# Kernel optimization log

Hardware: AMD Instinct MI355X
Metric: run time of the kernel (lower is better)

## Reference

```python
import jax, jax.numpy as jnp
import numpy as np

B, T, D = 4, 8160, 1024
N, H = 8, 128            # heads, units_per_head (D == N*H)
W = 12                   # block_size
LEFT_CTX = 13            # atten_left_context
L = LEFT_CTX - 1         # left context frames beyond current position
R = 0                    # atten_right_context
C = W + L + R            # context_size = 24
CAP = 50.0               # attention_logits_soft_capping


def _timing_signal(pos, channels):
    # sinusoidal embedding, channels even (1024)
    pos = pos.astype(jnp.float32)
    nt = channels // 2
    inc = np.log(10000.0) / max(nt - 1, 1)
    inv = jnp.exp(jnp.arange(nt, dtype=jnp.float32) * -inc)
    st = pos[:, :, None] * inv[None, None, :]
    return jnp.concatenate([jnp.sin(st), jnp.cos(st)], axis=2)


def _extract_block_context(x, block_size, left, right, pad_val):
    # x: [B, T, ...] -> [B, num_blocks, context_size, ...]
    pads = [(0, 0)] * x.ndim
    pads[1] = (left, right + block_size - 1)
    xp = jnp.pad(x, pads, constant_values=jnp.asarray(pad_val, x.dtype))
    frame_len = block_size + left + right
    num_frames = (xp.shape[1] - frame_len) // block_size + 1
    idx = jnp.arange(num_frames)[:, None] * block_size + jnp.arange(frame_len)[None, :]
    return jnp.take(xp, idx, axis=1)


def _convert_to_block(x, block_size):
    b, t = x.shape[0], x.shape[1]
    nb = t // block_size  # T chosen as multiple of block_size
    return x.reshape((b, nb, block_size) + x.shape[2:])


def setup_inputs() -> dict:
    key = jax.random.key(0)
    ks = jax.random.split(key, 6)
    x = jax.random.normal(ks[0], (B, T, D), dtype=jnp.float32)
    mask = jnp.ones((B, T), dtype=bool)
    i = jnp.arange(W)[:, None]
    j = jnp.arange(C)[None, :]
    causal_valid_mask = (j >= i) & (j - i <= L + R)  # [W, C]
    s = 1.0 / np.sqrt(D)
    wq = jax.random.normal(ks[1], (D, D), dtype=jnp.float32) * s
    wk = jax.random.normal(ks[2], (D, D), dtype=jnp.float32) * s
    wv = jax.random.normal(ks[3], (D, D), dtype=jnp.float32) * s
    pos_proj = jax.random.normal(ks[4], (D, N, H), dtype=jnp.float32) * s
    return {"x": x, "mask": mask, "causal_valid_mask": causal_valid_mask,
            "wq": wq, "wk": wk, "wv": wv, "pos_proj": pos_proj}


def reference(x, mask, causal_valid_mask, wq, wk, wv, pos_proj):
    b, t, d = x.shape
    u = t // W
    q = jnp.einsum('btd,df->btf', x, wq).reshape(b, t, N, H)
    k = jnp.einsum('btd,df->btf', x, wk).reshape(b, t, N, H)
    v = jnp.einsum('btd,df->btf', x, wv).reshape(b, t, N, H)

    q_blk = _convert_to_block(q, W) * (H ** -0.5)        # [B,U,W,N,H]
    k_ctx = _extract_block_context(k, W, L, R, 0.0)      # [B,U,C,N,H]
    v_ctx = _extract_block_context(v, W, L, R, 0.0)      # [B,U,C,N,H]

    # term A+C: content logits
    term_ac = jnp.einsum('BuwNH,BucNH->BNuwc', q_blk, k_ctx)

    # term B+D: relative position logits via skew trick
    pos = jnp.arange(L, -R - 1, -1)[None, :]             # [1, L+R+1]
    sin_emb = _timing_signal(pos, D)                     # [1, L+R+1, D]
    sin_emb = jnp.einsum('fd,dnh->fnh', sin_emb[0], pos_proj)  # [F,N,H]
    term_bd = jnp.einsum('BuwNH,FNH->BNuwF', q_blk, sin_emb)   # [B,N,U,W,F]
    term_bd = jnp.pad(term_bd, ((0, 0),) * 4 + ((0, C + 1 - (L + R + 1)),))
    term_bd = term_bd.reshape(b, N, u, W * (C + 1))[:, :, :, :W * C]
    term_bd = term_bd.reshape(b, N, u, W, C)

    logits = term_ac + term_bd
    logits = CAP * jnp.tanh(logits / CAP)

    mask_ctx = _extract_block_context(mask, W, L, R, False)    # [B,U,C]
    valid = mask_ctx[:, None, :, None, :] & causal_valid_mask[None, None, None, :, :]
    logits = jnp.where(valid, logits, jnp.asarray(-1e9, logits.dtype))
    probs = jax.nn.softmax(logits, axis=-1)              # [B,N,U,W,C]

    out = jnp.einsum('BNuwc,BucNH->BuwNH', probs, v_ctx)
    return out.reshape(b, u * W, N, H)[:, :t]            # [B,T,N,H]
```

## Files before the change

kernel.cpp:

```cpp
#include <hip/hip_runtime.h>
#include <cstdint>
#include <cstddef>


typedef __bf16 bf16_t;
typedef float  floatx4 __attribute__((ext_vector_type(4)));
typedef __bf16 bf16x8  __attribute__((ext_vector_type(8)));
typedef __bf16 bf16x4  __attribute__((ext_vector_type(4)));

#define GLDS16(gp, lp)                                                        \
  __builtin_amdgcn_global_load_lds(                                           \
      (const __attribute__((address_space(1))) void*)(gp),                    \
      (__attribute__((address_space(3))) void*)(lp), 16, 0, 0)

static constexpr int kT     = 8160;
static constexpr int kM     = 4 * kT;
static constexpr int kU     = kT / 12;
static constexpr int kNC    = 3200;

__global__ __launch_bounds__(256) void convert_x(const float* __restrict__ X,
                                                 bf16_t* __restrict__ Xb) {
  const size_t i = ((size_t)blockIdx.x * 256 + threadIdx.x) * 8;
  float4 a = *(const float4*)(X + i);
  float4 b = *(const float4*)(X + i + 4);
  bf16x8 o;
  o[0] = (bf16_t)a.x; o[1] = (bf16_t)a.y; o[2] = (bf16_t)a.z; o[3] = (bf16_t)a.w;
  o[4] = (bf16_t)b.x; o[5] = (bf16_t)b.y; o[6] = (bf16_t)b.z; o[7] = (bf16_t)b.w;
  *(bf16x8*)(Xb + i) = o;
}

__global__ __launch_bounds__(512) void posemb_k(const float* __restrict__ pp,
                                                float* __restrict__ pe) {
  __shared__ float st[1024];
  __shared__ float red[4][128];
  const int d   = blockIdx.x;
  const int fc  = blockIdx.y;
  const int tid = threadIdx.x;
  const float dpos = (float)d;
  for (int i = tid; i < 1024; i += 512) {
    int idx = i & 511;
    float freq = expf(-(float)idx * (9.2103403719761836f / 511.0f));
    float a = dpos * freq;
    st[i] = (i < 512) ? sinf(a) : cosf(a);
  }
  __syncthreads();
  const int part = tid >> 7;
  const int fl   = tid & 127;
  const int f    = fc * 128 + fl;
  float acc = 0.f;
  const int dd0 = part * 256;
  for (int dd = dd0; dd < dd0 + 256; ++dd)
    acc += st[dd] * pp[(size_t)dd * 1024 + f];
  red[part][fl] = acc;
  __syncthreads();
  if (tid < 128)
    pe[(size_t)d * 1024 + f] = red[0][fl] + red[1][fl] + red[2][fl] + red[3][fl];
}

__global__ __launch_bounds__(256) void transpose_w(const float* __restrict__ Wq,
                                                   const float* __restrict__ Wk,
                                                   const float* __restrict__ Wv,
                                                   bf16_t* __restrict__ Wt) {
  __shared__ float tile[64][65];
  const int g = blockIdx.z;
  const float* W = (g == 0) ? Wq : (g == 1) ? Wk : Wv;
  bf16_t* O = Wt + (size_t)g * 1024 * 1024;
  const int k0 = blockIdx.x * 64, n0 = blockIdx.y * 64;
  const int col = threadIdx.x & 63, r4 = threadIdx.x >> 6;
#pragma unroll
  for (int i = 0; i < 16; ++i) {
    int row = i * 4 + r4;
    tile[row][col] = W[(size_t)(k0 + row) * 1024 + n0 + col];
  }
  __syncthreads();
#pragma unroll
  for (int i = 0; i < 16; ++i) {
    int row = i * 4 + r4;
    O[(size_t)(n0 + row) * 1024 + k0 + col] = (bf16_t)tile[col][row];
  }
}

__global__ __launch_bounds__(256) void pe2w(const float* __restrict__ pe,
                                            bf16_t* __restrict__ Wt) {
  const int idx = blockIdx.x;
  const int tid = threadIdx.x;
  bf16_t* out = Wt + (size_t)(3072 + idx) * 1024;
  if (idx >= 104) {
    bf16x4 z = {};
    *(bf16x4*)(out + tid * 4) = z;
    return;
  }
  const int n = idx / 13, d = idx - n * 13;
  __shared__ float peh[128];
  if (tid < 128) peh[tid] = pe[(size_t)d * 1024 + n * 128 + tid];
  __syncthreads();
  float acc[4] = {};
  const bf16_t* wb = Wt + (size_t)(n * 128) * 1024 + tid * 4;
  for (int h = 0; h < 128; ++h) {
    bf16x4 w4 = *(const bf16x4*)(wb + (size_t)h * 1024);
    float s = peh[h];
    acc[0] += s * (float)w4[0];
    acc[1] += s * (float)w4[1];
    acc[2] += s * (float)w4[2];
    acc[3] += s * (float)w4[3];
  }
  bf16x4 o;
  o[0] = (bf16_t)acc[0]; o[1] = (bf16_t)acc[1];
  o[2] = (bf16_t)acc[2]; o[3] = (bf16_t)acc[3];
  *(bf16x4*)(out + tid * 4) = o;
}

__global__ __launch_bounds__(512, 2) void qkv_gemm(const bf16_t* __restrict__ X,
                                                   const bf16_t* __restrict__ Wt,
                                                   bf16_t* __restrict__ QKV) {
  __shared__ __align__(16) bf16_t lds[8][8192];

  const int flat = blockIdx.x;
  const int work = (flat & 7) * 208 + (flat >> 3);
  const int mt = work / 13, nt = work % 13;
  const int m0 = mt * 256, n0 = nt * 256;

  const int tid  = threadIdx.x;
  const int wave = tid >> 6;
  const int lane = tid & 63;
  const int wm   = wave >> 2;
  const int wn   = wave & 3;
  const int qd   = lane >> 4;
  const int lr   = lane & 15;

  const int rr  = tid >> 3;
  const int cg8 = ((tid & 7) ^ (rr & 7)) * 8;
  const bf16_t* aP[4];
  const bf16_t* bP[4];
  {
    int r2 = m0 + 128 + rr, r3 = m0 + 192 + rr;
    aP[0] = X + (size_t)(m0 + rr) * 1024 + cg8;
    aP[1] = X + (size_t)(m0 + 64 + rr) * 1024 + cg8;
    aP[2] = X + (size_t)(r2 < kM ? r2 : 0) * 1024 + cg8;
    aP[3] = X + (size_t)(r3 < kM ? r3 : 0) * 1024 + cg8;
    int s2 = n0 + 128 + rr, s3 = n0 + 192 + rr;
    bP[0] = Wt + (size_t)(n0 + rr) * 1024 + cg8;
    bP[1] = Wt + (size_t)(n0 + 64 + rr) * 1024 + cg8;
    bP[2] = Wt + (size_t)(s2 < kNC ? s2 : 0) * 1024 + cg8;
    bP[3] = Wt + (size_t)(s3 < kNC ? s3 : 0) * 1024 + cg8;
  }

#define STAGE_A(h, t)                                                          \
  do {                                                                         \
    bf16_t* d_ = &lds[((t) & 1) * 4 + (h)][wave * 512];                        \
    GLDS16(aP[2 * (h)]     + (size_t)(t) * 64, d_);                            \
    GLDS16(aP[2 * (h) + 1] + (size_t)(t) * 64, d_ + 4096);                     \
  } while (0)
#define STAGE_B(h, t)                                                          \
  do {                                                                         \
    bf16_t* d_ = &lds[((t) & 1) * 4 + 2 + (h)][wave * 512];                    \
    GLDS16(bP[2 * (h)]     + (size_t)(t) * 64, d_);                            \
    GLDS16(bP[2 * (h) + 1] + (size_t)(t) * 64, d_ + 4096);                     \
  } while (0)

  auto frag = [&](int slot, int r, int cb) -> bf16x8 {
    uint32_t off = (uint32_t)(r * 128 + cb) ^ (uint32_t)((r & 7) << 4);
    return *(const bf16x8*)((const char*)&lds[slot][0] + off);
  };

  floatx4 acc[8][4] = {};

  STAGE_A(0, 0); STAGE_A(1, 0); STAGE_B(0, 0); STAGE_B(1, 0);
  STAGE_B(0, 1); STAGE_B(1, 1);
  asm volatile("s_waitcnt vmcnt(4)" ::: "memory");
  __builtin_amdgcn_s_barrier();

  const int aslot0 = wm;
  const int bslot0 = 2 + (wn >> 1);
  const int brow0  = (wn & 1) * 64;

#pragma unroll 2
  for (int t = 0; t < 16; ++t) {
    const int par = (t & 1) * 4;
    bf16x8 bfrag[4][2];
#pragma unroll
    for (int p = 0; p < 4; ++p) {
      if (p == 0) {
#pragma unroll
        for (int in = 0; in < 4; ++in)
#pragma unroll
          for (int k2 = 0; k2 < 2; ++k2)
            bfrag[in][k2] =
                frag(par + bslot0, brow0 + in * 16 + lr, k2 * 64 + qd * 16);
      }
      bf16x8 afrag[2][2];
#pragma unroll
      for (int i = 0; i < 2; ++i)
#pragma unroll
        for (int k2 = 0; k2 < 2; ++k2)
          afrag[i][k2] =
              frag(par + aslot0, (2 * p + i) * 16 + lr, k2 * 64 + qd * 16);

      if (p == 0)      { if (t < 15) STAGE_A(0, t + 1); }
      else if (p == 1) { if (t < 15) STAGE_A(1, t + 1); }
      else if (p == 2) { if (t < 14) STAGE_B(0, t + 2); }
      else             { if (t < 14) STAGE_B(1, t + 2); }

      if (p == 3) {
        if (t < 14) asm volatile("s_waitcnt vmcnt(4)" ::: "memory");
        else        asm volatile("s_waitcnt vmcnt(0)" ::: "memory");
      }
      __builtin_amdgcn_s_barrier();
      asm volatile("s_waitcnt lgkmcnt(0)" ::: "memory");
      __builtin_amdgcn_sched_barrier(0);

      __builtin_amdgcn_s_setprio(1);
#pragma unroll
      for (int i = 0; i < 2; ++i)
#pragma unroll
        for (int in = 0; in < 4; ++in)
#pragma unroll
          for (int k2 = 0; k2 < 2; ++k2)
            acc[2 * p + i][in] = __builtin_amdgcn_mfma_f32_16x16x32_bf16(
                afrag[i][k2], bfrag[in][k2], acc[2 * p + i][in], 0, 0, 0);
      __builtin_amdgcn_s_setprio(0);
      __builtin_amdgcn_sched_barrier(0);
      __builtin_amdgcn_s_barrier();
    }
  }
#undef STAGE_A
#undef STAGE_B

  const int mBase = m0 + wm * 128 + qd * 4;
  const int nBase = n0 + wn * 64 + lr;
  if (m0 + 256 <= kM && n0 + 256 <= kNC) {
#pragma unroll
    for (int im = 0; im < 8; ++im)
#pragma unroll
      for (int in = 0; in < 4; ++in)
#pragma unroll
        for (int r = 0; r < 4; ++r)
          QKV[(size_t)(mBase + im * 16 + r) * kNC + nBase + in * 16] =
              (bf16_t)acc[im][in][r];
  } else {
#pragma unroll
    for (int im = 0; im < 8; ++im)
#pragma unroll
      for (int in = 0; in < 4; ++in)
#pragma unroll
        for (int r = 0; r < 4; ++r) {
          int m = mBase + im * 16 + r;
          int n = nBase + in * 16;
          if (m < kM && n < kNC)
            QKV[(size_t)m * kNC + n] = (bf16_t)acc[im][in][r];
        }
  }
}

__global__ __launch_bounds__(256) void qk_soft(const bf16_t* __restrict__ QKV,
                                               float* __restrict__ Pg) {
  __shared__ __align__(16) bf16_t Ks[80 * 128];
  __shared__ float qpes[64 * 16];

  const int flat  = blockIdx.x;
  const int work  = (flat & 7) * 544 + (flat >> 3);
  const int strip = work >> 5;
  const int rest  = work & 31;
  const int n     = rest >> 2;
  const int b     = rest & 3;
  const int u0    = strip * 5;
  const int t0    = u0 * 12 - 12;
  const size_t bbase = (size_t)b * kT;
  const int bn    = b * 8 + n;
  const int tid  = threadIdx.x;
  const int mi   = tid >> 6;
  const int lane = tid & 63;
  const int qd   = lane >> 4;
  const int lr   = lane & 15;

  bf16x8 aQ[4];
  {
    int tq = u0 * 12 + mi * 16 + lr;
    if (tq > kT - 1) tq = kT - 1;
    const bf16_t* qg = QKV + (bbase + tq) * kNC + n * 128;
#pragma unroll
    for (int kk = 0; kk < 4; ++kk)
      aQ[kk] = *(const bf16x8*)(qg + kk * 32 + qd * 8);
  }

  for (int i = tid; i < 80 * 16; i += 256) {
    int row = i >> 4, ch = i & 15;
    int kt = t0 + row;
    bf16x8 k8 = {};
    if (kt >= 0 && kt < kT)
      k8 = *(const bf16x8*)(QKV + (bbase + kt) * kNC + 1024 + n * 128 + ch * 8);
    int idx = (row * 128 + ch * 8) ^ ((row & 7) << 3);
    *(bf16x8*)(Ks + idx) = k8;
  }
  for (int i = tid; i < 780; i += 256) {
    int m = i / 13, d = i - m * 13;
    qpes[m * 16 + d] =
        (float)QKV[(bbase + (u0 * 12 + m)) * kNC + 3072 + n * 13 + d];
  }
  __syncthreads();

  floatx4 sAcc[2] = {};
#pragma unroll
  for (int ci = 0; ci < 2; ++ci) {
    int krow = (mi + ci) * 16 + lr;
#pragma unroll
    for (int kk = 0; kk < 4; ++kk) {
      int idx = (krow * 128 + kk * 32 + qd * 8) ^ ((krow & 7) << 3);
      bf16x8 bK = *(const bf16x8*)(Ks + idx);
      sAcc[ci] = __builtin_amdgcn_mfma_f32_16x16x32_bf16(aQ[kk], bK, sAcc[ci], 0, 0, 0);
    }
  }

#pragma unroll
  for (int r = 0; r < 4; ++r) {
    const int m = mi * 16 + qd * 4 + r;
    float e[2];
#pragma unroll
    for (int ci = 0; ci < 2; ++ci) {
      int c = (mi + ci) * 16 + lr;
      int d = m + 12 - c;
      int kt = t0 + c;
      bool v = (d >= 0) && (d <= 12) && (kt >= 0) && (m < 60);
      int qidx = m * 16 + (v ? d : 0);
      float s = (sAcc[ci][r] + qpes[qidx]) * 0.0017677669529663689f;
      float t2 = __expf(2.0f * s);
      float th = 1.0f - 2.0f / (t2 + 1.0f);
      e[ci] = v ? __expf(50.0f * th) : 0.0f;
    }
    float sm = e[0] + e[1];
    sm += __shfl_xor(sm, 1);
    sm += __shfl_xor(sm, 2);
    sm += __shfl_xor(sm, 4);
    sm += __shfl_xor(sm, 8);
    float iv = 1.0f / sm;
#pragma unroll
    for (int ci = 0; ci < 2; ++ci) {
      int c = (mi + ci) * 16 + lr;
      int d = m + 12 - c;
      if (m < 60 && d >= 0 && d <= 12)
        Pg[((size_t)bn * kT + (u0 * 12 + m)) * 16 + d] = e[ci] * iv;
    }
  }
}

__global__ __launch_bounds__(256) void pv_k(const bf16_t* __restrict__ QKV,
                                            const float* __restrict__ Pg,
                                            float* __restrict__ OUT) {
  __shared__ float Vs[60 * 132];
  __shared__ float ps[48 * 16];

  const int flat = blockIdx.x;
  const int work = (flat & 7) * 680 + (flat >> 3);
  const int bn = work / 170, ts = work % 170;
  const int b  = bn >> 3, n = bn & 7;
  const int t1 = ts * 48;
  const size_t bbase = (size_t)b * kT;
  const int tid = threadIdx.x;

  for (int i = tid; i < 60 * 16; i += 256) {
    int r = i >> 4, ch = i & 15;
    int kt = t1 - 12 + r;
    int vo = r * 132 + ch * 8;
    if (kt < 0) {
      float4 z = {};
      *(float4*)(Vs + vo) = z; *(float4*)(Vs + vo + 4) = z;
    } else {
      bf16x8 v8 = *(const bf16x8*)(QKV + (bbase + kt) * kNC + 2048 + n * 128 + ch * 8);
      float4 vl = { (float)v8[0], (float)v8[1], (float)v8[2], (float)v8[3] };
      float4 vh = { (float)v8[4], (float)v8[5], (float)v8[6], (float)v8[7] };
      *(float4*)(Vs + vo) = vl; *(float4*)(Vs + vo + 4) = vh;
    }
  }
  if (tid < 192) {
    int r = tid >> 2, q4 = tid & 3;
    float4 p4 = *(const float4*)(Pg + ((size_t)bn * kT + t1 + r) * 16 + q4 * 4);
    *(float4*)(ps + r * 16 + q4 * 4) = p4;
  }
  __syncthreads();

  for (int i = tid; i < 48 * 32; i += 256) {
    int lt = i >> 5, c4 = i & 31;
    const float* pw = ps + lt * 16;
    float4 acc = {};
#pragma unroll
    for (int d = 0; d <= 12; ++d) {
      float pd = pw[d];
      float4 v4 = *(const float4*)(Vs + (lt + 12 - d) * 132 + c4 * 4);
      acc.x += pd * v4.x; acc.y += pd * v4.y;
      acc.z += pd * v4.z; acc.w += pd * v4.w;
    }
    *(float4*)(OUT + (bbase + t1 + lt) * 1024 + n * 128 + c4 * 4) = acc;
  }
}

extern "C" void kernel_launch(void* const* d_in, const int* in_sizes, int n_in,
                              void* d_out, int out_size, void* d_ws, size_t ws_size,
                              hipStream_t stream) {
  const float* x  = (const float*)d_in[0];
  const float* wq = (const float*)d_in[3];
  const float* wk = (const float*)d_in[4];
  const float* wv = (const float*)d_in[5];
  const float* pp = (const float*)d_in[6];

  char* ws = (char*)d_ws;
  float*  pe  = (float*)ws;
  bf16_t* Wt  = (bf16_t*)(ws + (1u << 16));
  bf16_t* Xb  = (bf16_t*)(ws + (1u << 16) + 8u * 1024 * 1024);
  bf16_t* QKV = (bf16_t*)(ws + (1u << 16) + 8u * 1024 * 1024 +
                          (size_t)kM * 1024 * 2);
  float* Pg = (float*)Xb;
  float* out = (float*)d_out;

  convert_x<<<kM * 1024 / (256 * 8), 256, 0, stream>>>(x, Xb);
  posemb_k<<<dim3(13, 8), 512, 0, stream>>>(pp, pe);
  transpose_w<<<dim3(16, 16, 3), 256, 0, stream>>>(wq, wk, wv, Wt);
  pe2w<<<128, 256, 0, stream>>>(pe, Wt);
  qkv_gemm<<<1664, 512, 0, stream>>>(Xb, Wt, QKV);
  qk_soft<<<4352, 256, 0, stream>>>(QKV, Pg);
  pv_k<<<5440, 256, 0, stream>>>(QKV, Pg, out);
}
```

Baseline: 588.5 us.

## Store Q/K/V in head-major layout and pack positional logits separately

After: 584.3 us. Within noise of the previous version (-0.7%).

```diff
diff --git a/kernel.cpp b/kernel.cpp
--- a/kernel.cpp
+++ b/kernel.cpp
@@ -17,6 +17,7 @@
 static constexpr int kM     = 4 * kT;
 static constexpr int kU     = kT / 12;
 static constexpr int kNC    = 3200;
+static constexpr size_t kArrE = (size_t)4 * 8 * 8160 * 128;
 
 __global__ __launch_bounds__(256) void convert_x(const float* __restrict__ X,
                                                  bf16_t* __restrict__ Xb) {
@@ -49,6 +50,7 @@
   const int f    = fc * 128 + fl;
   float acc = 0.f;
   const int dd0 = part * 256;
+#pragma unroll 8
   for (int dd = dd0; dd < dd0 + 256; ++dd)
     acc += st[dd] * pp[(size_t)dd * 1024 + f];
   red[part][fl] = acc;
@@ -96,6 +98,7 @@
   __syncthreads();
   float acc[4] = {};
   const bf16_t* wb = Wt + (size_t)(n * 128) * 1024 + tid * 4;
+#pragma unroll 8
   for (int h = 0; h < 128; ++h) {
     bf16x4 w4 = *(const bf16x4*)(wb + (size_t)h * 1024);
     float s = peh[h];
@@ -112,7 +115,7 @@
 
 __global__ __launch_bounds__(512, 2) void qkv_gemm(const bf16_t* __restrict__ X,
                                                    const bf16_t* __restrict__ Wt,
-                                                   bf16_t* __restrict__ QKV) {
+                                                   bf16_t* __restrict__ O) {
   __shared__ __align__(16) bf16_t lds[8][8192];
 
   const int flat = blockIdx.x;
@@ -228,31 +231,52 @@
 
   const int mBase = m0 + wm * 128 + qd * 4;
   const int nBase = n0 + wn * 64 + lr;
-  if (m0 + 256 <= kM && n0 + 256 <= kNC) {
+  bf16_t* QPE = O + 3 * kArrE;
+  if (n0 < 3072) {
+    const bool interior = (m0 + 256 <= kM);
 #pragma unroll
     for (int im = 0; im < 8; ++im)
 #pragma unroll
-      for (int in = 0; in < 4; ++in)
-#pragma unroll
-        for (int r = 0; r < 4; ++r)
-          QKV[(size_t)(mBase + im * 16 + r) * kNC + nBase + in * 16] =
+      for (int r = 0; r < 4; ++r) {
+        const int mm = mBase + im * 16 + r;
+        if (!interior && mm >= kM) continue;
+        const int bb = mm / 8160;
+        const int tt = mm - bb * 8160;
+#pragma unroll
+        for (int in = 0; in < 4; ++in) {
+          const int nc = nBase + in * 16;
+          const int sec = nc >> 10;
+          const int nh  = (nc >> 7) & 7;
+          const int h   = nc & 127;
+          O[(size_t)sec * kArrE +
+            (((size_t)(bb * 8 + nh) * 8160 + tt) << 7) + h] =
               (bf16_t)acc[im][in][r];
+        }
+      }
   } else {
 #pragma unroll
     for (int im = 0; im < 8; ++im)
 #pragma unroll
-      for (int in = 0; in < 4; ++in)
-#pragma unroll
-        for (int r = 0; r < 4; ++r) {
-          int m = mBase + im * 16 + r;
-          int n = nBase + in * 16;
-          if (m < kM && n < kNC)
-            QKV[(size_t)m * kNC + n] = (bf16_t)acc[im][in][r];
+      for (int r = 0; r < 4; ++r) {
+        const int mm = mBase + im * 16 + r;
+        if (mm >= kM) continue;
+        const int bb = mm / 8160;
+        const int tt = mm - bb * 8160;
+#pragma unroll
+        for (int in = 0; in < 4; ++in) {
+          const int idx = nBase + in * 16 - 3072;
+          if (idx < 104) {
+            const int nh = idx / 13;
+            const int d  = idx - nh * 13;
+            QPE[(((size_t)(bb * 8 + nh) * 8160 + tt) << 4) + d] =
+                (bf16_t)acc[im][in][r];
+          }
         }
-  }
-}
-
-__global__ __launch_bounds__(256) void qk_soft(const bf16_t* __restrict__ QKV,
+      }
+  }
+}
+
+__global__ __launch_bounds__(256) void qk_soft(const bf16_t* __restrict__ O,
                                                float* __restrict__ Pg) {
   __shared__ __align__(16) bf16_t Ks[80 * 128];
   __shared__ float qpes[64 * 16];
@@ -265,19 +289,22 @@
   const int b     = rest & 3;
   const int u0    = strip * 5;
   const int t0    = u0 * 12 - 12;
-  const size_t bbase = (size_t)b * kT;
   const int bn    = b * 8 + n;
+  const size_t hb = (size_t)bn * kT;
   const int tid  = threadIdx.x;
   const int mi   = tid >> 6;
   const int lane = tid & 63;
   const int qd   = lane >> 4;
   const int lr   = lane & 15;
 
+  const bf16_t* KH  = O + kArrE;
+  const bf16_t* QPE = O + 3 * kArrE;
+
   bf16x8 aQ[4];
   {
     int tq = u0 * 12 + mi * 16 + lr;
     if (tq > kT - 1) tq = kT - 1;
-    const bf16_t* qg = QKV + (bbase + tq) * kNC + n * 128;
+    const bf16_t* qg = O + (hb + tq) * 128;
 #pragma unroll
     for (int kk = 0; kk < 4; ++kk)
       aQ[kk] = *(const bf16x8*)(qg + kk * 32 + qd * 8);
@@ -288,14 +315,16 @@
     int kt = t0 + row;
     bf16x8 k8 = {};
     if (kt >= 0 && kt < kT)
-      k8 = *(const bf16x8*)(QKV + (bbase + kt) * kNC + 1024 + n * 128 + ch * 8);
+      k8 = *(const bf16x8*)(KH + (hb + kt) * 128 + ch * 8);
     int idx = (row * 128 + ch * 8) ^ ((row & 7) << 3);
     *(bf16x8*)(Ks + idx) = k8;
   }
-  for (int i = tid; i < 780; i += 256) {
-    int m = i / 13, d = i - m * 13;
-    qpes[m * 16 + d] =
-        (float)QKV[(bbase + (u0 * 12 + m)) * kNC + 3072 + n * 13 + d];
+  if (tid < 120) {
+    int m = tid >> 1, hx = tid & 1;
+    bf16x8 q8 = *(const bf16x8*)(QPE + (hb + (u0 * 12 + m)) * 16 + hx * 8);
+#pragma unroll
+    for (int j = 0; j < 8; ++j)
+      qpes[m * 16 + hx * 8 + j] = (float)q8[j];
   }
   __syncthreads();
 
@@ -343,7 +372,7 @@
   }
 }
 
-__global__ __launch_bounds__(256) void pv_k(const bf16_t* __restrict__ QKV,
+__global__ __launch_bounds__(256) void pv_k(const bf16_t* __restrict__ O,
                                             const float* __restrict__ Pg,
                                             float* __restrict__ OUT) {
   __shared__ float Vs[60 * 132];
@@ -354,8 +383,11 @@
   const int bn = work / 170, ts = work % 170;
   const int b  = bn >> 3, n = bn & 7;
   const int t1 = ts * 48;
+  const size_t hb = (size_t)bn * kT;
   const size_t bbase = (size_t)b * kT;
   const int tid = threadIdx.x;
+
+  const bf16_t* VH = O + 2 * kArrE;
 
   for (int i = tid; i < 60 * 16; i += 256) {
     int r = i >> 4, ch = i & 15;
@@ -365,7 +397,7 @@
       float4 z = {};
       *(float4*)(Vs + vo) = z; *(float4*)(Vs + vo + 4) = z;
     } else {
-      bf16x8 v8 = *(const bf16x8*)(QKV + (bbase + kt) * kNC + 2048 + n * 128 + ch * 8);
+      bf16x8 v8 = *(const bf16x8*)(VH + (hb + kt) * 128 + ch * 8);
       float4 vl = { (float)v8[0], (float)v8[1], (float)v8[2], (float)v8[3] };
       float4 vh = { (float)v8[4], (float)v8[5], (float)v8[6], (float)v8[7] };
       *(float4*)(Vs + vo) = vl; *(float4*)(Vs + vo + 4) = vh;
@@ -406,7 +438,7 @@
   float*  pe  = (float*)ws;
   bf16_t* Wt  = (bf16_t*)(ws + (1u << 16));
   bf16_t* Xb  = (bf16_t*)(ws + (1u << 16) + 8u * 1024 * 1024);
-  bf16_t* QKV = (bf16_t*)(ws + (1u << 16) + 8u * 1024 * 1024 +
+  bf16_t* OH  = (bf16_t*)(ws + (1u << 16) + 8u * 1024 * 1024 +
                           (size_t)kM * 1024 * 2);
   float* Pg = (float*)Xb;
   float* out = (float*)d_out;
@@ -415,7 +447,7 @@
   posemb_k<<<dim3(13, 8), 512, 0, stream>>>(pp, pe);
   transpose_w<<<dim3(16, 16, 3), 256, 0, stream>>>(wq, wk, wv, Wt);
   pe2w<<<128, 256, 0, stream>>>(pe, Wt);
-  qkv_gemm<<<1664, 512, 0, stream>>>(Xb, Wt, QKV);
-  qk_soft<<<4352, 256, 0, stream>>>(QKV, Pg);
-  pv_k<<<5440, 256, 0, stream>>>(QKV, Pg, out);
-}
+  qkv_gemm<<<1664, 512, 0, stream>>>(Xb, Wt, OH);
+  qk_soft<<<4352, 256, 0, stream>>>(OH, Pg);
+  pv_k<<<5440, 256, 0, stream>>>(OH, Pg, out);
+}
```
